# Kernel optimization log

Hardware: AMD Instinct MI355X
Metric: run time of the kernel (lower is better)

The kernel has to match this reference:

```python
import jax, jax.numpy as jnp
import numpy as np
from jax import lax

B, T, F = 2048, 512, 8
C = 16   # conv out channels
H = 10   # lstm hidden size


def setup_inputs() -> dict:
    key = jax.random.key(0)
    ks = jax.random.split(key, 12)
    s_conv = 1.0 / np.sqrt(F * 3)
    s1 = 1.0 / np.sqrt(H)
    inp = {
        'x': jax.random.normal(ks[0], (B, T, F), dtype=jnp.float32),
        'conv_w': jax.random.uniform(ks[1], (C, F, 3), jnp.float32, -s_conv, s_conv),
        'conv_b': jax.random.uniform(ks[2], (C,), jnp.float32, -s_conv, s_conv),
        'w_ih1': jax.random.uniform(ks[3], (4 * H, C), jnp.float32, -s1, s1),
        'w_hh1': jax.random.uniform(ks[4], (4 * H, H), jnp.float32, -s1, s1),
        'b_ih1': jax.random.uniform(ks[5], (4 * H,), jnp.float32, -s1, s1),
        'b_hh1': jax.random.uniform(ks[6], (4 * H,), jnp.float32, -s1, s1),
        'w_ih2': jax.random.uniform(ks[7], (4 * H, H), jnp.float32, -s1, s1),
        'w_hh2': jax.random.uniform(ks[8], (4 * H, H), jnp.float32, -s1, s1),
        'b_ih2': jax.random.uniform(ks[9], (4 * H,), jnp.float32, -s1, s1),
        'b_hh2': jax.random.uniform(ks[9], (4 * H,), jnp.float32, -s1, s1),
        'lin_w': jax.random.uniform(ks[10], (1, H), jnp.float32, -s1, s1),
        'lin_b': jax.random.uniform(ks[11], (1,), jnp.float32, -s1, s1),
    }
    return inp


def _lstm(seq, w_ih, w_hh, b_ih, b_hh):
    # seq: [B, T, D] -> hidden stream [B, T, H]; PyTorch gate order i,f,g,o.
    xg = jnp.einsum('btd,gd->btg', seq, w_ih) + (b_ih + b_hh)  # [B,T,4H]
    h0 = jnp.zeros((seq.shape[0], H), seq.dtype)

    def step(carry, xg_t):
        h, c = carry
        g = xg_t + h @ w_hh.T
        i, f, gg, o = jnp.split(g, 4, axis=-1)
        c = jax.nn.sigmoid(f) * c + jax.nn.sigmoid(i) * jnp.tanh(gg)
        h = jax.nn.sigmoid(o) * jnp.tanh(c)
        return (h, c), h

    _, hs = lax.scan(step, (h0, h0), jnp.swapaxes(xg, 0, 1))  # [T,B,H]
    return jnp.swapaxes(hs, 0, 1)


def reference(x, conv_w, conv_b, w_ih1, w_hh1, b_ih1, b_hh1,
              w_ih2, w_hh2, b_ih2, b_hh2, lin_w, lin_b):
    # conv1d over time, padding=1 keeps length (dropout is identity in eval)
    xc = jnp.transpose(x, (0, 2, 1))  # [B,F,T]
    y = lax.conv_general_dilated(xc, conv_w, window_strides=(1,),
                                 padding=[(1, 1)],
                                 dimension_numbers=('NCH', 'OIH', 'NCH'))
    y = jax.nn.relu(y + conv_b[None, :, None])
    y = jnp.transpose(y, (0, 2, 1))  # [B,T,C]
    h1 = _lstm(y, w_ih1, w_hh1, b_ih1, b_hh1)
    h2 = _lstm(h1, w_ih2, w_hh2, b_ih2, b_hh2)
    last = h2[:, -1, :]  # [B,H]
    return jax.nn.sigmoid(last @ lin_w.T + lin_b)  # [B,1]
```

## Files before the change

kernel.cpp:

```cpp
#include <hip/hip_runtime.h>

#define TT 512
#define FF 8
#define CC 16
#define HH 10
#define G4 40

__device__ __forceinline__ float rl(float v, int k){
    return __int_as_float(__builtin_amdgcn_readlane(__float_as_int(v), k));
}
__device__ __forceinline__ float sigf(float z){
    return __builtin_amdgcn_rcpf(1.f + __expf(-z));
}
__device__ __forceinline__ float tanh_f(float z){
    return 1.f - 2.f * __builtin_amdgcn_rcpf(1.f + __expf(2.f * z));
}
#define PIN(v) asm volatile("" : "+v"(v))

#define CONV_Y(Y) do{                                                                              \
    float a0 = cb, a1 = 0.f;                                                                       \
    a0 = fmaf(w0a.x, cw0,  a0); a1 = fmaf(w1a.x, cw1,  a1); a0 = fmaf(w2a.x, cw2,  a0);            \
    a1 = fmaf(w0a.y, cw3,  a1); a0 = fmaf(w1a.y, cw4,  a0); a1 = fmaf(w2a.y, cw5,  a1);            \
    a0 = fmaf(w0a.z, cw6,  a0); a1 = fmaf(w1a.z, cw7,  a1); a0 = fmaf(w2a.z, cw8,  a0);            \
    a1 = fmaf(w0a.w, cw9,  a1); a0 = fmaf(w1a.w, cw10, a0); a1 = fmaf(w2a.w, cw11, a1);            \
    a0 = fmaf(w0b.x, cw12, a0); a1 = fmaf(w1b.x, cw13, a1); a0 = fmaf(w2b.x, cw14, a0);            \
    a1 = fmaf(w0b.y, cw15, a1); a0 = fmaf(w1b.y, cw16, a0); a1 = fmaf(w2b.y, cw17, a1);            \
    a0 = fmaf(w0b.z, cw18, a0); a1 = fmaf(w1b.z, cw19, a1); a0 = fmaf(w2b.z, cw20, a0);            \
    a1 = fmaf(w0b.w, cw21, a1); a0 = fmaf(w1b.w, cw22, a0); a1 = fmaf(w2b.w, cw23, a1);            \
    Y = fmaxf(a0 + a1, 0.f);                                                                       \
}while(0)

#define H1BCAST                                                                                    \
    const float hs0=rl(h1,0), hs1=rl(h1,1), hs2=rl(h1,2), hs3=rl(h1,3), hs4=rl(h1,4),              \
                hs5=rl(h1,5), hs6=rl(h1,6), hs7=rl(h1,7), hs8=rl(h1,8), hs9=rl(h1,9);

#define LAYER2 do{                                                                                 \
    float d0 = b2, d1 = 0.f;                                                                       \
    d0 = fmaf(hs0, wi2_0, d0);  d1 = fmaf(hs1, wi2_1, d1);                                         \
    d0 = fmaf(hs2, wi2_2, d0);  d1 = fmaf(hs3, wi2_3, d1);                                         \
    d0 = fmaf(hs4, wi2_4, d0);  d1 = fmaf(hs5, wi2_5, d1);                                         \
    d0 = fmaf(hs6, wi2_6, d0);  d1 = fmaf(hs7, wi2_7, d1);                                         \
    d0 = fmaf(hs8, wi2_8, d0);  d1 = fmaf(hs9, wi2_9, d1);                                         \
    d0 = fmaf(rl(h2,0), wh2_0, d0);  d1 = fmaf(rl(h2,1), wh2_1, d1);                               \
    d0 = fmaf(rl(h2,2), wh2_2, d0);  d1 = fmaf(rl(h2,3), wh2_3, d1);                               \
    d0 = fmaf(rl(h2,4), wh2_4, d0);  d1 = fmaf(rl(h2,5), wh2_5, d1);                               \
    d0 = fmaf(rl(h2,6), wh2_6, d0);  d1 = fmaf(rl(h2,7), wh2_7, d1);                               \
    d0 = fmaf(rl(h2,8), wh2_8, d0);  d1 = fmaf(rl(h2,9), wh2_9, d1);                               \
    const float g2  = d0 + d1;                                                                     \
    const float sg2 = sigf(g2 * zM);                                                               \
    const float act2 = fmaf(aA, sg2, aB);                                                          \
    const float ai2 = __shfl(act2, u,      64);                                                    \
    const float af2 = __shfl(act2, u + 10, 64);                                                    \
    const float ag2 = __shfl(act2, u + 20, 64);                                                    \
    const float ao2 = __shfl(act2, u + 30, 64);                                                    \
    c2 = fmaf(af2, c2, ai2 * ag2);                                                                 \
    h2 = ao2 * tanh_f(c2);                                                                         \
}while(0)

#define LAYER1(YV) do{                                                                             \
    float e0 = b1, e1 = 0.f;                                                                       \
    e0 = fmaf(rl(YV,0),  wi0,  e0);  e1 = fmaf(rl(YV,1),  wi1,  e1);                               \
    e0 = fmaf(rl(YV,2),  wi2,  e0);  e1 = fmaf(rl(YV,3),  wi3,  e1);                               \
    e0 = fmaf(rl(YV,4),  wi4,  e0);  e1 = fmaf(rl(YV,5),  wi5,  e1);                               \
    e0 = fmaf(rl(YV,6),  wi6,  e0);  e1 = fmaf(rl(YV,7),  wi7,  e1);                               \
    e0 = fmaf(rl(YV,8),  wi8,  e0);  e1 = fmaf(rl(YV,9),  wi9,  e1);                               \
    e0 = fmaf(rl(YV,10), wi10, e0);  e1 = fmaf(rl(YV,11), wi11, e1);                               \
    e0 = fmaf(rl(YV,12), wi12, e0);  e1 = fmaf(rl(YV,13), wi13, e1);                               \
    e0 = fmaf(rl(YV,14), wi14, e0);  e1 = fmaf(rl(YV,15), wi15, e1);                               \
    e0 = fmaf(hs0, wh1_0, e0);  e1 = fmaf(hs1, wh1_1, e1);                                         \
    e0 = fmaf(hs2, wh1_2, e0);  e1 = fmaf(hs3, wh1_3, e1);                                         \
    e0 = fmaf(hs4, wh1_4, e0);  e1 = fmaf(hs5, wh1_5, e1);                                         \
    e0 = fmaf(hs6, wh1_6, e0);  e1 = fmaf(hs7, wh1_7, e1);                                         \
    e0 = fmaf(hs8, wh1_8, e0);  e1 = fmaf(hs9, wh1_9, e1);                                         \
    const float g1  = e0 + e1;                                                                     \
    const float sg1 = sigf(g1 * zM);                                                               \
    const float act1 = fmaf(aA, sg1, aB);                                                          \
    const float ai1 = __shfl(act1, u,      64);                                                    \
    const float af1 = __shfl(act1, u + 10, 64);                                                    \
    const float ag1 = __shfl(act1, u + 20, 64);                                                    \
    const float ao1 = __shfl(act1, u + 30, 64);                                                    \
    c1 = fmaf(af1, c1, ai1 * ag1);                                                                 \
    h1n = ao1 * tanh_f(c1);                                                                        \
}while(0)

__global__ __launch_bounds__(64, 1)
void lstm_fused(const float* __restrict__ x,
                const float* __restrict__ conv_w, const float* __restrict__ conv_b,
                const float* __restrict__ w_ih1,  const float* __restrict__ w_hh1,
                const float* __restrict__ b_ih1,  const float* __restrict__ b_hh1,
                const float* __restrict__ w_ih2,  const float* __restrict__ w_hh2,
                const float* __restrict__ b_ih2,  const float* __restrict__ b_hh2,
                const float* __restrict__ lin_w,  const float* __restrict__ lin_b,
                float* __restrict__ out)
{
    __shared__ float wl[64][73];

    const int lane  = threadIdx.x;
    const int batch = blockIdx.x;
    const int grow  = (lane < G4) ? lane : (G4-1);
    const int q     = grow / 10;
    const int u     = grow - q * 10;
    const int ch    = lane & 15;
    const bool isG  = (q == 2);
    float zM = isG ? 2.f : 1.f;
    float aA = isG ? 2.f : 1.f;
    float aB = isG ? -1.f : 0.f;
    PIN(zM); PIN(aA); PIN(aB);

    {
        float* mr = wl[lane];
        const float* cwp = conv_w + ch*24;
        #pragma unroll
        for (int m = 0; m < 24; ++m) mr[m] = cwp[m];
        const float* wip = w_ih1 + grow*CC;
        #pragma unroll
        for (int m = 0; m < CC; ++m) mr[24+m] = wip[m];
        const float* q1 = w_hh1 + grow*HH;
        const float* q2 = w_ih2 + grow*HH;
        const float* q3 = w_hh2 + grow*HH;
        #pragma unroll
        for (int m = 0; m < HH; ++m){ mr[40+m]=q1[m]; mr[50+m]=q2[m]; mr[60+m]=q3[m]; }
        mr[70] = b_ih1[grow] + b_hh1[grow];
        mr[71] = b_ih2[grow] + b_hh2[grow];
        mr[72] = conv_b[ch];
    }
    __syncthreads();
    const float* mr = wl[lane];

    float cw0=mr[0],  cw1=mr[1],  cw2=mr[2],  cw3=mr[3],  cw4=mr[4],  cw5=mr[5];
    float cw6=mr[6],  cw7=mr[7],  cw8=mr[8],  cw9=mr[9],  cw10=mr[10],cw11=mr[11];
    float cw12=mr[12],cw13=mr[13],cw14=mr[14],cw15=mr[15],cw16=mr[16],cw17=mr[17];
    float cw18=mr[18],cw19=mr[19],cw20=mr[20],cw21=mr[21],cw22=mr[22],cw23=mr[23];
    PIN(cw0);PIN(cw1);PIN(cw2);PIN(cw3);PIN(cw4);PIN(cw5);PIN(cw6);PIN(cw7);
    PIN(cw8);PIN(cw9);PIN(cw10);PIN(cw11);PIN(cw12);PIN(cw13);PIN(cw14);PIN(cw15);
    PIN(cw16);PIN(cw17);PIN(cw18);PIN(cw19);PIN(cw20);PIN(cw21);PIN(cw22);PIN(cw23);

    float wi0=mr[24], wi1=mr[25], wi2=mr[26], wi3=mr[27];
    float wi4=mr[28], wi5=mr[29], wi6=mr[30], wi7=mr[31];
    float wi8=mr[32], wi9=mr[33], wi10=mr[34],wi11=mr[35];
    float wi12=mr[36],wi13=mr[37],wi14=mr[38],wi15=mr[39];
    PIN(wi0);PIN(wi1);PIN(wi2);PIN(wi3);PIN(wi4);PIN(wi5);PIN(wi6);PIN(wi7);
    PIN(wi8);PIN(wi9);PIN(wi10);PIN(wi11);PIN(wi12);PIN(wi13);PIN(wi14);PIN(wi15);

    float wh1_0=mr[40],wh1_1=mr[41],wh1_2=mr[42],wh1_3=mr[43],wh1_4=mr[44];
    float wh1_5=mr[45],wh1_6=mr[46],wh1_7=mr[47],wh1_8=mr[48],wh1_9=mr[49];
    PIN(wh1_0);PIN(wh1_1);PIN(wh1_2);PIN(wh1_3);PIN(wh1_4);
    PIN(wh1_5);PIN(wh1_6);PIN(wh1_7);PIN(wh1_8);PIN(wh1_9);

    float wi2_0=mr[50],wi2_1=mr[51],wi2_2=mr[52],wi2_3=mr[53],wi2_4=mr[54];
    float wi2_5=mr[55],wi2_6=mr[56],wi2_7=mr[57],wi2_8=mr[58],wi2_9=mr[59];
    PIN(wi2_0);PIN(wi2_1);PIN(wi2_2);PIN(wi2_3);PIN(wi2_4);
    PIN(wi2_5);PIN(wi2_6);PIN(wi2_7);PIN(wi2_8);PIN(wi2_9);

    float wh2_0=mr[60],wh2_1=mr[61],wh2_2=mr[62],wh2_3=mr[63],wh2_4=mr[64];
    float wh2_5=mr[65],wh2_6=mr[66],wh2_7=mr[67],wh2_8=mr[68],wh2_9=mr[69];
    PIN(wh2_0);PIN(wh2_1);PIN(wh2_2);PIN(wh2_3);PIN(wh2_4);
    PIN(wh2_5);PIN(wh2_6);PIN(wh2_7);PIN(wh2_8);PIN(wh2_9);

    float b1 = mr[70]; PIN(b1);
    float b2 = mr[71]; PIN(b2);
    float cb = mr[72]; PIN(cb);

    const float* xb = x + (size_t)batch * (TT*FF);

    float h1 = 0.f, c1 = 0.f, h2 = 0.f, c2 = 0.f, h1n;

    float4 w0a = make_float4(0.f,0.f,0.f,0.f), w0b = w0a;
    float4 w1a = *(const float4*)(xb + 0);
    float4 w1b = *(const float4*)(xb + 4);
    float4 w2a = *(const float4*)(xb + 8);
    float4 w2b = *(const float4*)(xb + 12);

    {
        float y0; CONV_Y(y0);
        H1BCAST;
        LAYER1(y0);
        h1 = h1n;
    }
    w0a = w1a; w0b = w1b; w1a = w2a; w1b = w2b;
    w2a = *(const float4*)(xb + 16);
    w2b = *(const float4*)(xb + 20);

    #pragma unroll 3
    for (int t = 1; t < TT; ++t){
        float4 nxa = make_float4(0.f,0.f,0.f,0.f), nxb = nxa;
        if (t + 2 < TT){
            const float* p = xb + (t+2)*FF;
            nxa = *(const float4*)p;
            nxb = *(const float4*)(p + 4);
        }
        float y; CONV_Y(y);
        {
            H1BCAST;
            LAYER2;
            LAYER1(y);
        }
        h1 = h1n;
        w0a = w1a; w0b = w1b; w1a = w2a; w1b = w2b; w2a = nxa; w2b = nxb;
    }
    {
        H1BCAST;
        LAYER2;
    }

    float part = (lane < HH) ? h2 * lin_w[grow] : 0.f;
    #pragma unroll
    for (int off = 8; off > 0; off >>= 1) part += __shfl_xor(part, off, 16);
    if (lane == 0) out[batch] = sigf(part + lin_b[0]);
}

extern "C" void kernel_launch(void* const* d_in, const int* in_sizes, int n_in,
                              void* d_out, int out_size, void* d_ws, size_t ws_size,
                              hipStream_t stream) {
    const float* x      = (const float*)d_in[0];
    const float* conv_w = (const float*)d_in[1];
    const float* conv_b = (const float*)d_in[2];
    const float* w_ih1  = (const float*)d_in[3];
    const float* w_hh1  = (const float*)d_in[4];
    const float* b_ih1  = (const float*)d_in[5];
    const float* b_hh1  = (const float*)d_in[6];
    const float* w_ih2  = (const float*)d_in[7];
    const float* w_hh2  = (const float*)d_in[8];
    const float* b_ih2  = (const float*)d_in[9];
    const float* b_hh2  = (const float*)d_in[10];
    const float* lin_w  = (const float*)d_in[11];
    const float* lin_b  = (const float*)d_in[12];
    float* out = (float*)d_out;

    lstm_fused<<<dim3(2048), dim3(64), 0, stream>>>(
        x, conv_w, conv_b, w_ih1, w_hh1, b_ih1, b_hh1,
        w_ih2, w_hh2, b_ih2, b_hh2, lin_w, lin_b, out);
}
```

Before: 271.2 us.

## Split conv and input projection into a parallel precompute kernel before recurrence

Adds a kernel that computes the conv and layer-1 input-gate projections for all timesteps in parallel and stores them in a workspace buffer. A second kernel then runs only the recurrent LSTM steps, reading precomputed gates. Gate rows are also remapped so that the four gates of a hidden unit sit in one lane quad, and DPP quad broadcasts replace shuffles. This shortens the serial per-step path but adds a large global write and read of the gate tensor, and it falls back to the fused kernel if the workspace is too small.

```diff
diff --git a/kernel.cpp b/kernel.cpp
--- a/kernel.cpp
+++ b/kernel.cpp
@@ -16,6 +16,11 @@
     return 1.f - 2.f * __builtin_amdgcn_rcpf(1.f + __expf(2.f * z));
 }
 #define PIN(v) asm volatile("" : "+v"(v))
+
+template<int Q>
+__device__ __forceinline__ float quadb(float v){
+    return __int_as_float(__builtin_amdgcn_mov_dpp(__float_as_int(v), Q * 0x55, 0xf, 0xf, false));
+}
 
 #define CONV_Y(Y) do{                                                                              \
     float a0 = cb, a1 = 0.f;                                                                       \
@@ -29,6 +34,208 @@
     a1 = fmaf(w0b.w, cw21, a1); a0 = fmaf(w1b.w, cw22, a0); a1 = fmaf(w2b.w, cw23, a1);            \
     Y = fmaxf(a0 + a1, 0.f);                                                                       \
 }while(0)
+
+__global__ __launch_bounds__(64, 1)
+void conv_xg(const float* __restrict__ x,
+             const float* __restrict__ conv_w, const float* __restrict__ conv_b,
+             const float* __restrict__ w_ih1,  const float* __restrict__ b_ih1,
+             const float* __restrict__ b_hh1,
+             float* __restrict__ xg)
+{
+    __shared__ float wl[64][43];
+    const int lane = threadIdx.x;
+    const int b    = blockIdx.x;
+    const int ch   = lane & 15;
+    const int g    = lane >> 4;
+    const int u_c  = (lane < G4) ? (lane >> 2) : 9;
+    const int q    = lane & 3;
+    const int r    = q * 10 + u_c;
+
+    {
+        float* mr_ = wl[lane];
+        const float* cwp = conv_w + ch*24;
+        #pragma unroll
+        for (int m = 0; m < 24; ++m) mr_[m] = cwp[m];
+        const float* wip = w_ih1 + r*CC;
+        #pragma unroll
+        for (int k = 0; k < CC; ++k) mr_[24+k] = wip[k];
+        mr_[40] = b_ih1[r] + b_hh1[r];
+        mr_[41] = conv_b[ch];
+    }
+    __syncthreads();
+    const float* mr = wl[lane];
+
+    float cw0=mr[0],  cw1=mr[1],  cw2=mr[2],  cw3=mr[3],  cw4=mr[4],  cw5=mr[5];
+    float cw6=mr[6],  cw7=mr[7],  cw8=mr[8],  cw9=mr[9],  cw10=mr[10],cw11=mr[11];
+    float cw12=mr[12],cw13=mr[13],cw14=mr[14],cw15=mr[15],cw16=mr[16],cw17=mr[17];
+    float cw18=mr[18],cw19=mr[19],cw20=mr[20],cw21=mr[21],cw22=mr[22],cw23=mr[23];
+    PIN(cw0);PIN(cw1);PIN(cw2);PIN(cw3);PIN(cw4);PIN(cw5);PIN(cw6);PIN(cw7);
+    PIN(cw8);PIN(cw9);PIN(cw10);PIN(cw11);PIN(cw12);PIN(cw13);PIN(cw14);PIN(cw15);
+    PIN(cw16);PIN(cw17);PIN(cw18);PIN(cw19);PIN(cw20);PIN(cw21);PIN(cw22);PIN(cw23);
+    float wi0=mr[24], wi1=mr[25], wi2=mr[26], wi3=mr[27];
+    float wi4=mr[28], wi5=mr[29], wi6=mr[30], wi7=mr[31];
+    float wi8=mr[32], wi9=mr[33], wi10=mr[34],wi11=mr[35];
+    float wi12=mr[36],wi13=mr[37],wi14=mr[38],wi15=mr[39];
+    PIN(wi0);PIN(wi1);PIN(wi2);PIN(wi3);PIN(wi4);PIN(wi5);PIN(wi6);PIN(wi7);
+    PIN(wi8);PIN(wi9);PIN(wi10);PIN(wi11);PIN(wi12);PIN(wi13);PIN(wi14);PIN(wi15);
+    float b1r = mr[40]; PIN(b1r);
+    float cb  = mr[41]; PIN(cb);
+
+    const float* xb  = x  + (size_t)b * (TT*FF);
+    float*       xgb = xg + (size_t)b * (TT*G4);
+    const float4 z4 = make_float4(0.f,0.f,0.f,0.f);
+
+    #pragma unroll 1
+    for (int tb = 0; tb < TT/4; ++tb){
+        const int tq = tb*4 + g;
+        float4 w0a, w0b, w1a, w1b, w2a, w2b;
+        if (tq == 0){ w0a = z4; w0b = z4; }
+        else { const float* p = xb + (tq-1)*FF; w0a = *(const float4*)p; w0b = *(const float4*)(p+4); }
+        { const float* p = xb + tq*FF; w1a = *(const float4*)p; w1b = *(const float4*)(p+4); }
+        if (tq + 1 < TT){ const float* p = xb + (tq+1)*FF; w2a = *(const float4*)p; w2b = *(const float4*)(p+4); }
+        else { w2a = z4; w2b = z4; }
+
+        float y; CONV_Y(y);
+
+        #pragma unroll
+        for (int s = 0; s < 4; ++s){
+            float e0 = b1r, e1 = 0.f;
+            e0 = fmaf(rl(y, s*16+0),  wi0,  e0);  e1 = fmaf(rl(y, s*16+1),  wi1,  e1);
+            e0 = fmaf(rl(y, s*16+2),  wi2,  e0);  e1 = fmaf(rl(y, s*16+3),  wi3,  e1);
+            e0 = fmaf(rl(y, s*16+4),  wi4,  e0);  e1 = fmaf(rl(y, s*16+5),  wi5,  e1);
+            e0 = fmaf(rl(y, s*16+6),  wi6,  e0);  e1 = fmaf(rl(y, s*16+7),  wi7,  e1);
+            e0 = fmaf(rl(y, s*16+8),  wi8,  e0);  e1 = fmaf(rl(y, s*16+9),  wi9,  e1);
+            e0 = fmaf(rl(y, s*16+10), wi10, e0);  e1 = fmaf(rl(y, s*16+11), wi11, e1);
+            e0 = fmaf(rl(y, s*16+12), wi12, e0);  e1 = fmaf(rl(y, s*16+13), wi13, e1);
+            e0 = fmaf(rl(y, s*16+14), wi14, e0);  e1 = fmaf(rl(y, s*16+15), wi15, e1);
+            if (lane < G4) xgb[(tb*4+s)*G4 + lane] = e0 + e1;
+        }
+    }
+}
+
+#define BH1B                                                                     \
+    const float hs0=rl(h1,0),  hs1=rl(h1,4),  hs2=rl(h1,8),  hs3=rl(h1,12),      \
+                hs4=rl(h1,16), hs5=rl(h1,20), hs6=rl(h1,24), hs7=rl(h1,28),      \
+                hs8=rl(h1,32), hs9=rl(h1,36);
+
+#define BL2 do{                                                                  \
+    float d0 = b2, d1 = 0.f;                                                     \
+    d0 = fmaf(hs0, wi2_0, d0);  d1 = fmaf(hs1, wi2_1, d1);                       \
+    d0 = fmaf(hs2, wi2_2, d0);  d1 = fmaf(hs3, wi2_3, d1);                       \
+    d0 = fmaf(hs4, wi2_4, d0);  d1 = fmaf(hs5, wi2_5, d1);                       \
+    d0 = fmaf(hs6, wi2_6, d0);  d1 = fmaf(hs7, wi2_7, d1);                       \
+    d0 = fmaf(hs8, wi2_8, d0);  d1 = fmaf(hs9, wi2_9, d1);                       \
+    d0 = fmaf(rl(h2,0),  wh2_0, d0);  d1 = fmaf(rl(h2,4),  wh2_1, d1);           \
+    d0 = fmaf(rl(h2,8),  wh2_2, d0);  d1 = fmaf(rl(h2,12), wh2_3, d1);           \
+    d0 = fmaf(rl(h2,16), wh2_4, d0);  d1 = fmaf(rl(h2,20), wh2_5, d1);           \
+    d0 = fmaf(rl(h2,24), wh2_6, d0);  d1 = fmaf(rl(h2,28), wh2_7, d1);           \
+    d0 = fmaf(rl(h2,32), wh2_8, d0);  d1 = fmaf(rl(h2,36), wh2_9, d1);           \
+    const float g2  = d0 + d1;                                                   \
+    const float sg2 = sigf(g2 * zM);                                             \
+    const float act2 = fmaf(aA, sg2, aB);                                        \
+    const float ai2 = quadb<0>(act2);                                            \
+    const float af2 = quadb<1>(act2);                                            \
+    const float ag2 = quadb<2>(act2);                                            \
+    const float ao2 = quadb<3>(act2);                                            \
+    c2 = fmaf(af2, c2, ai2 * ag2);                                               \
+    h2 = ao2 * tanh_f(c2);                                                       \
+}while(0)
+
+#define BL1(XGV) do{                                                             \
+    float e0 = (XGV), e1 = 0.f;                                                  \
+    e0 = fmaf(hs0, wh1_0, e0);  e1 = fmaf(hs1, wh1_1, e1);                       \
+    e0 = fmaf(hs2, wh1_2, e0);  e1 = fmaf(hs3, wh1_3, e1);                       \
+    e0 = fmaf(hs4, wh1_4, e0);  e1 = fmaf(hs5, wh1_5, e1);                       \
+    e0 = fmaf(hs6, wh1_6, e0);  e1 = fmaf(hs7, wh1_7, e1);                       \
+    e0 = fmaf(hs8, wh1_8, e0);  e1 = fmaf(hs9, wh1_9, e1);                       \
+    const float g1  = e0 + e1;                                                   \
+    const float sg1 = sigf(g1 * zM);                                             \
+    const float act1 = fmaf(aA, sg1, aB);                                        \
+    const float ai1 = quadb<0>(act1);                                            \
+    const float af1 = quadb<1>(act1);                                            \
+    const float ag1 = quadb<2>(act1);                                            \
+    const float ao1 = quadb<3>(act1);                                            \
+    c1 = fmaf(af1, c1, ai1 * ag1);                                               \
+    h1n = ao1 * tanh_f(c1);                                                      \
+}while(0)
+
+__global__ __launch_bounds__(64, 1)
+void lstm_seq(const float* __restrict__ xg,
+              const float* __restrict__ w_hh1,
+              const float* __restrict__ w_ih2,  const float* __restrict__ w_hh2,
+              const float* __restrict__ b_ih2,  const float* __restrict__ b_hh2,
+              const float* __restrict__ lin_w,  const float* __restrict__ lin_b,
+              float* __restrict__ out)
+{
+    __shared__ float wl[64][31];
+    const int lane  = threadIdx.x;
+    const int batch = blockIdx.x;
+    const int u_c   = (lane < G4) ? (lane >> 2) : 9;
+    const int q     = lane & 3;
+    const int r     = q * 10 + u_c;
+    const bool isG  = (q == 2);
+    float zM = isG ? 2.f : 1.f;
+    float aA = isG ? 2.f : 1.f;
+    float aB = isG ? -1.f : 0.f;
+    PIN(zM); PIN(aA); PIN(aB);
+
+    {
+        float* mr_ = wl[lane];
+        const float* q1 = w_hh1 + r*HH;
+        const float* q2 = w_ih2 + r*HH;
+        const float* q3 = w_hh2 + r*HH;
+        #pragma unroll
+        for (int m = 0; m < HH; ++m){ mr_[m]=q1[m]; mr_[10+m]=q2[m]; mr_[20+m]=q3[m]; }
+        mr_[30] = b_ih2[r] + b_hh2[r];
+    }
+    __syncthreads();
+    const float* mr = wl[lane];
+
+    float wh1_0=mr[0], wh1_1=mr[1], wh1_2=mr[2], wh1_3=mr[3], wh1_4=mr[4];
+    float wh1_5=mr[5], wh1_6=mr[6], wh1_7=mr[7], wh1_8=mr[8], wh1_9=mr[9];
+    PIN(wh1_0);PIN(wh1_1);PIN(wh1_2);PIN(wh1_3);PIN(wh1_4);
+    PIN(wh1_5);PIN(wh1_6);PIN(wh1_7);PIN(wh1_8);PIN(wh1_9);
+    float wi2_0=mr[10],wi2_1=mr[11],wi2_2=mr[12],wi2_3=mr[13],wi2_4=mr[14];
+    float wi2_5=mr[15],wi2_6=mr[16],wi2_7=mr[17],wi2_8=mr[18],wi2_9=mr[19];
+    PIN(wi2_0);PIN(wi2_1);PIN(wi2_2);PIN(wi2_3);PIN(wi2_4);
+    PIN(wi2_5);PIN(wi2_6);PIN(wi2_7);PIN(wi2_8);PIN(wi2_9);
+    float wh2_0=mr[20],wh2_1=mr[21],wh2_2=mr[22],wh2_3=mr[23],wh2_4=mr[24];
+    float wh2_5=mr[25],wh2_6=mr[26],wh2_7=mr[27],wh2_8=mr[28],wh2_9=mr[29];
+    PIN(wh2_0);PIN(wh2_1);PIN(wh2_2);PIN(wh2_3);PIN(wh2_4);
+    PIN(wh2_5);PIN(wh2_6);PIN(wh2_7);PIN(wh2_8);PIN(wh2_9);
+    float b2 = mr[30]; PIN(b2);
+
+    const float* xp = xg + (size_t)batch * (TT*G4) + ((lane < G4) ? lane : (G4-1));
+
+    float h1 = 0.f, c1 = 0.f, h2 = 0.f, c2 = 0.f, h1n;
+
+    float xgv = xp[0];
+    {
+        BH1B;
+        BL1(xgv);
+        h1 = h1n;
+    }
+    float xgn = xp[G4];
+
+    #pragma unroll 2
+    for (int t = 1; t < TT; ++t){
+        const float xgc = xgn;
+        const int tn = (t + 1 < TT) ? (t + 1) : (TT - 1);
+        xgn = xp[(size_t)tn * G4];
+        BH1B;
+        BL2;
+        BL1(xgc);
+        h1 = h1n;
+    }
+    { BH1B; BL2; }
+
+    float part = (q == 0 && lane < G4) ? h2 * lin_w[u_c] : 0.f;
+    part += __shfl_xor(part, 4,  64);
+    part += __shfl_xor(part, 8,  64);
+    part += __shfl_xor(part, 16, 64);
+    part += __shfl_xor(part, 32, 64);
+    if (lane == 0) out[batch] = sigf(part + lin_b[0]);
+}
 
 #define H1BCAST                                                                                    \
     const float hs0=rl(h1,0), hs1=rl(h1,1), hs2=rl(h1,2), hs3=rl(h1,3), hs4=rl(h1,4),              \
@@ -94,7 +301,6 @@
                 float* __restrict__ out)
 {
     __shared__ float wl[64][73];
-
     const int lane  = threadIdx.x;
     const int batch = blockIdx.x;
     const int grow  = (lane < G4) ? lane : (G4-1);
@@ -108,21 +314,21 @@
     PIN(zM); PIN(aA); PIN(aB);
 
     {
-        float* mr = wl[lane];
+        float* mr_ = wl[lane];
         const float* cwp = conv_w + ch*24;
         #pragma unroll
-        for (int m = 0; m < 24; ++m) mr[m] = cwp[m];
+        for (int m = 0; m < 24; ++m) mr_[m] = cwp[m];
         const float* wip = w_ih1 + grow*CC;
         #pragma unroll
-        for (int m = 0; m < CC; ++m) mr[24+m] = wip[m];
+        for (int m = 0; m < CC; ++m) mr_[24+m] = wip[m];
         const float* q1 = w_hh1 + grow*HH;
         const float* q2 = w_ih2 + grow*HH;
         const float* q3 = w_hh2 + grow*HH;
         #pragma unroll
-        for (int m = 0; m < HH; ++m){ mr[40+m]=q1[m]; mr[50+m]=q2[m]; mr[60+m]=q3[m]; }
-        mr[70] = b_ih1[grow] + b_hh1[grow];
-        mr[71] = b_ih2[grow] + b_hh2[grow];
-        mr[72] = conv_b[ch];
+        for (int m = 0; m < HH; ++m){ mr_[40+m]=q1[m]; mr_[50+m]=q2[m]; mr_[60+m]=q3[m]; }
+        mr_[70] = b_ih1[grow] + b_hh1[grow];
+        mr_[71] = b_ih2[grow] + b_hh2[grow];
+        mr_[72] = conv_b[ch];
     }
     __syncthreads();
     const float* mr = wl[lane];
@@ -131,38 +337,19 @@
     float cw6=mr[6],  cw7=mr[7],  cw8=mr[8],  cw9=mr[9],  cw10=mr[10],cw11=mr[11];
     float cw12=mr[12],cw13=mr[13],cw14=mr[14],cw15=mr[15],cw16=mr[16],cw17=mr[17];
     float cw18=mr[18],cw19=mr[19],cw20=mr[20],cw21=mr[21],cw22=mr[22],cw23=mr[23];
-    PIN(cw0);PIN(cw1);PIN(cw2);PIN(cw3);PIN(cw4);PIN(cw5);PIN(cw6);PIN(cw7);
-    PIN(cw8);PIN(cw9);PIN(cw10);PIN(cw11);PIN(cw12);PIN(cw13);PIN(cw14);PIN(cw15);
-    PIN(cw16);PIN(cw17);PIN(cw18);PIN(cw19);PIN(cw20);PIN(cw21);PIN(cw22);PIN(cw23);
-
     float wi0=mr[24], wi1=mr[25], wi2=mr[26], wi3=mr[27];
     float wi4=mr[28], wi5=mr[29], wi6=mr[30], wi7=mr[31];
     float wi8=mr[32], wi9=mr[33], wi10=mr[34],wi11=mr[35];
     float wi12=mr[36],wi13=mr[37],wi14=mr[38],wi15=mr[39];
-    PIN(wi0);PIN(wi1);PIN(wi2);PIN(wi3);PIN(wi4);PIN(wi5);PIN(wi6);PIN(wi7);
-    PIN(wi8);PIN(wi9);PIN(wi10);PIN(wi11);PIN(wi12);PIN(wi13);PIN(wi14);PIN(wi15);
-
     float wh1_0=mr[40],wh1_1=mr[41],wh1_2=mr[42],wh1_3=mr[43],wh1_4=mr[44];
     float wh1_5=mr[45],wh1_6=mr[46],wh1_7=mr[47],wh1_8=mr[48],wh1_9=mr[49];
-    PIN(wh1_0);PIN(wh1_1);PIN(wh1_2);PIN(wh1_3);PIN(wh1_4);
-    PIN(wh1_5);PIN(wh1_6);PIN(wh1_7);PIN(wh1_8);PIN(wh1_9);
-
     float wi2_0=mr[50],wi2_1=mr[51],wi2_2=mr[52],wi2_3=mr[53],wi2_4=mr[54];
     float wi2_5=mr[55],wi2_6=mr[56],wi2_7=mr[57],wi2_8=mr[58],wi2_9=mr[59];
-    PIN(wi2_0);PIN(wi2_1);PIN(wi2_2);PIN(wi2_3);PIN(wi2_4);
-    PIN(wi2_5);PIN(wi2_6);PIN(wi2_7);PIN(wi2_8);PIN(wi2_9);
-
     float wh2_0=mr[60],wh2_1=mr[61],wh2_2=mr[62],wh2_3=mr[63],wh2_4=mr[64];
     float wh2_5=mr[65],wh2_6=mr[66],wh2_7=mr[67],wh2_8=mr[68],wh2_9=mr[69];
-    PIN(wh2_0);PIN(wh2_1);PIN(wh2_2);PIN(wh2_3);PIN(wh2_4);
-    PIN(wh2_5);PIN(wh2_6);PIN(wh2_7);PIN(wh2_8);PIN(wh2_9);
-
-    float b1 = mr[70]; PIN(b1);
-    float b2 = mr[71]; PIN(b2);
-    float cb = mr[72]; PIN(cb);
+    float b1 = mr[70], b2 = mr[71], cb = mr[72];
 
     const float* xb = x + (size_t)batch * (TT*FF);
-
     float h1 = 0.f, c1 = 0.f, h2 = 0.f, c2 = 0.f, h1n;
 
     float4 w0a = make_float4(0.f,0.f,0.f,0.f), w0b = w0a;
@@ -198,10 +385,7 @@
         h1 = h1n;
         w0a = w1a; w0b = w1b; w1a = w2a; w1b = w2b; w2a = nxa; w2b = nxb;
     }
-    {
-        H1BCAST;
-        LAYER2;
-    }
+    { H1BCAST; LAYER2; }
 
     float part = (lane < HH) ? h2 * lin_w[grow] : 0.f;
     #pragma unroll
@@ -227,7 +411,18 @@
     const float* lin_b  = (const float*)d_in[12];
     float* out = (float*)d_out;
 
-    lstm_fused<<<dim3(2048), dim3(64), 0, stream>>>(
-        x, conv_w, conv_b, w_ih1, w_hh1, b_ih1, b_hh1,
-        w_ih2, w_hh2, b_ih2, b_hh2, lin_w, lin_b, out);
-}
+    const int NB = 2048;
+    const size_t XG_BYTES = (size_t)NB * TT * G4 * sizeof(float);
+
+    if (ws_size >= XG_BYTES){
+        float* xgws = (float*)d_ws;
+        conv_xg<<<dim3(NB), dim3(64), 0, stream>>>(
+            x, conv_w, conv_b, w_ih1, b_ih1, b_hh1, xgws);
+        lstm_seq<<<dim3(NB), dim3(64), 0, stream>>>(
+            xgws, w_hh1, w_ih2, w_hh2, b_ih2, b_hh2, lin_w, lin_b, out);
+    } else {
+        lstm_fused<<<dim3(NB), dim3(64), 0, stream>>>(
+            x, conv_w, conv_b, w_ih1, w_hh1, b_ih1, b_hh1,
+            w_ih2, w_hh2, b_ih2, b_hh2, lin_w, lin_b, out);
+    }
+}
```

After: 295.5 us. 8.9% more time.
